# Optimization experiments

Hardware: AMD Instinct MI355X
Metric: run time of the kernel (lower is better)

Reference implementation:

```python
import jax, jax.numpy as jnp
import numpy as np


def euler_xyz_to_matrix(angles):
    # pytorch3d euler_angles_to_matrix(angles, 'XYZ') = R_X(a0) @ R_Y(a1) @ R_Z(a2)
    ax, ay, az = angles[..., 0], angles[..., 1], angles[..., 2]
    cx, sx = jnp.cos(ax), jnp.sin(ax)
    cy, sy = jnp.cos(ay), jnp.sin(ay)
    cz, sz = jnp.cos(az), jnp.sin(az)
    one = jnp.ones_like(ax)
    zero = jnp.zeros_like(ax)
    Rx = jnp.stack([one, zero, zero, zero, cx, -sx, zero, sx, cx], axis=-1).reshape(*ax.shape, 3, 3)
    Ry = jnp.stack([cy, zero, sy, zero, one, zero, -sy, zero, cy], axis=-1).reshape(*ax.shape, 3, 3)
    Rz = jnp.stack([cz, -sz, zero, sz, cz, zero, zero, zero, one], axis=-1).reshape(*ax.shape, 3, 3)
    return Rx @ Ry @ Rz


def chamfer_bidir(x, y):
    # x, y: [R, I, N, 3]. Squared-distance chamfer, mean point reduction, per (R,I) batch.
    x2 = jnp.sum(x * x, axis=-1)  # [R,I,N]
    y2 = jnp.sum(y * y, axis=-1)  # [R,I,N]
    # d2[r,i,n,m] = |x_n - y_m|^2
    d2 = x2[..., :, None] + y2[..., None, :] - 2.0 * jnp.einsum('rind,rimd->rinm', x, y)
    cham_x = jnp.mean(jnp.min(d2, axis=-1), axis=-1)  # x -> nearest y
    cham_y = jnp.mean(jnp.min(d2, axis=-2), axis=-1)  # y -> nearest x
    return cham_x + cham_y  # [R, I]


def setup_inputs() -> dict:
    key = jax.random.key(0)
    k1, k2, k3, k4 = jax.random.split(key, 4)
    R, I, N = 4, 16, 2048
    source_points = jax.random.normal(k1, (R, I, N, 3), dtype=jnp.float32)
    target_points = jax.random.normal(k2, (I, N, 3), dtype=jnp.float32)
    rotation = 0.1 * jax.random.normal(k3, (R, I, 3), dtype=jnp.float32)
    translation = 0.1 * jax.random.normal(k4, (R, I, 3), dtype=jnp.float32)
    scale = jnp.ones((R, I), dtype=jnp.float32)
    return {
        'source_points': source_points,
        'target_points': target_points,
        'rotation': rotation,
        'translation': translation,
        'scale': scale,
    }


def reference(source_points, target_points, rotation, translation, scale):
    R, I, N, _ = source_points.shape
    rot = euler_xyz_to_matrix(rotation)  # [R,I,3,3]
    # Transform per original: 4x4 matrix with rows [:3,:] scaled by `scale`,
    # so p' = scale * (rot @ p + translation).
    transformed = scale[..., None, None] * (
        jnp.einsum('rind,rikd->rink', source_points, rot) + translation[..., None, :]
    )  # [R,I,N,3]
    # target_points [I,N,3] broadcast to [R,I,N,3] (original repeats along R)
    target = jnp.broadcast_to(target_points[None], transformed.shape)
    # original calls chamfer_distance(target, transformed): x=target, y=transformed
    return chamfer_bidir(target, transformed)  # [R, I]
```

## Files before the change

kernel.cpp:

```cpp
#include <hip/hip_runtime.h>
#include <math.h>

#define RDIM 4
#define IDIM 16
#define NPAIR 64
#define NPTS 2048
#define THREADS 256
#define ROWSB 256
#define RBLK (NPTS / ROWSB)
#define TILES (NPTS / 32)
#define PSPLIT 4
#define ONEBF 0x3F80u

typedef __attribute__((ext_vector_type(8))) short bf16x8;
typedef __attribute__((ext_vector_type(16))) float f32x16;
typedef __attribute__((ext_vector_type(4))) float f32x4;

__device__ __forceinline__ float min3f(float a, float b, float c) {
    return fminf(a, fminf(b, c));
}

__device__ __forceinline__ unsigned int f2bf(float f) {
    union { float f; unsigned int u; } v; v.f = f;
    return (v.u + 0x7FFFu + ((v.u >> 16) & 1u)) >> 16;
}
__device__ __forceinline__ float bf2f(unsigned int h) {
    union { unsigned int u; float f; } v; v.u = h << 16; return v.f;
}

__device__ __forceinline__ void make_rot(const float* __restrict__ rotv, int pair,
                                         float& r00, float& r01, float& r02,
                                         float& r10, float& r11, float& r12,
                                         float& r20, float& r21, float& r22) {
    const float ax = rotv[pair * 3 + 0];
    const float ay = rotv[pair * 3 + 1];
    const float az = rotv[pair * 3 + 2];
    float sx, cx, sy, cy, sz, cz;
    sincosf(ax, &sx, &cx);
    sincosf(ay, &sy, &cy);
    sincosf(az, &sz, &cz);
    r00 = cy * cz;                r01 = -cy * sz;               r02 = sy;
    r10 = cx * sz + sx * sy * cz; r11 = cx * cz - sx * sy * sz; r12 = -sx * cy;
    r20 = sx * sz - cx * sy * cz; r21 = sx * cz + cx * sy * sz; r22 = cx * cy;
}

__device__ __forceinline__ uint4 brec(float v0, float v1, float v2) {
    const float b0 = -2.0f * v0, b1 = -2.0f * v1, b2 = -2.0f * v2;
    const unsigned int h0 = f2bf(b0), h1 = f2bf(b1), h2 = f2bf(b2);
    const unsigned int l0 = f2bf(b0 - bf2f(h0));
    const unsigned int l1 = f2bf(b1 - bf2f(h1));
    const unsigned int l2 = f2bf(b2 - bf2f(h2));
    const float n2 = v0 * v0 + v1 * v1 + v2 * v2;
    const unsigned int nh = f2bf(n2), nl = f2bf(n2 - bf2f(nh));
    return make_uint4(h0 | (h1 << 16), h2 | (l0 << 16), l1 | (l2 << 16), nh | (nl << 16));
}
__device__ __forceinline__ void arec(float q0, float q1, float q2, uint4& a0, uint4& a1) {
    const unsigned int h0 = f2bf(q0), h1 = f2bf(q1), h2 = f2bf(q2);
    const unsigned int l0 = f2bf(q0 - bf2f(h0));
    const unsigned int l1 = f2bf(q1 - bf2f(h1));
    const unsigned int l2 = f2bf(q2 - bf2f(h2));
    a0 = make_uint4(h0 | (h1 << 16), h2 | (l0 << 16), l1 | (l2 << 16), ONEBF);
    a1 = make_uint4(l0 | (l1 << 16), l2 | (h0 << 16), h1 | (h2 << 16), ONEBF << 16);
}

__global__ __launch_bounds__(THREADS)
void prep(const float* __restrict__ src, const float* __restrict__ tgt,
          const float* __restrict__ rotv, const float* __restrict__ trav,
          const float* __restrict__ scal,
          uint4* __restrict__ Yb, uint4* __restrict__ Ya,
          uint4* __restrict__ Xb, uint4* __restrict__ Xa,
          float* __restrict__ out)
{
    const int b   = blockIdx.x;
    const int seg = blockIdx.y;
    const int tid = threadIdx.x;
    if (b == 0 && seg == 0 && tid < NPAIR) out[tid] = 0.0f;
    const int m0  = seg * (NPTS / PSPLIT);
    if (b < NPAIR) {
        const int pair = b;
        float r00, r01, r02, r10, r11, r12, r20, r21, r22;
        make_rot(rotv, pair, r00, r01, r02, r10, r11, r12, r20, r21, r22);
        const float t0 = trav[pair * 3 + 0];
        const float t1 = trav[pair * 3 + 1];
        const float t2 = trav[pair * 3 + 2];
        const float s  = scal[pair];
        const float* __restrict__ srcp = src + (size_t)pair * NPTS * 3;
#pragma unroll
        for (int u = 0; u < NPTS / THREADS / PSPLIT; ++u) {
            const int m = m0 + u * THREADS + tid;
            const float p0 = srcp[m * 3 + 0];
            const float p1 = srcp[m * 3 + 1];
            const float p2 = srcp[m * 3 + 2];
            const float y0 = s * fmaf(r00, p0, fmaf(r01, p1, fmaf(r02, p2, t0)));
            const float y1 = s * fmaf(r10, p0, fmaf(r11, p1, fmaf(r12, p2, t1)));
            const float y2 = s * fmaf(r20, p0, fmaf(r21, p1, fmaf(r22, p2, t2)));
            Yb[(size_t)pair * NPTS + m] = brec(y0, y1, y2);
            uint4 a0, a1;
            arec(y0, y1, y2, a0, a1);
            Ya[((size_t)pair * NPTS + m) * 2 + 0] = a0;
            Ya[((size_t)pair * NPTS + m) * 2 + 1] = a1;
        }
    } else {
        const int i = b - NPAIR;
        const float* __restrict__ tgtp = tgt + (size_t)i * NPTS * 3;
#pragma unroll
        for (int u = 0; u < NPTS / THREADS / PSPLIT; ++u) {
            const int m = m0 + u * THREADS + tid;
            const float x0 = tgtp[m * 3 + 0];
            const float x1 = tgtp[m * 3 + 1];
            const float x2 = tgtp[m * 3 + 2];
            Xb[(size_t)i * NPTS + m] = brec(x0, x1, x2);
            uint4 a0, a1;
            arec(x0, x1, x2, a0, a1);
            Xa[((size_t)i * NPTS + m) * 2 + 0] = a0;
            Xa[((size_t)i * NPTS + m) * 2 + 1] = a1;
        }
    }
}

__global__ __launch_bounds__(THREADS, 3)
void chamfer_main(const uint4* __restrict__ Yb, const uint4* __restrict__ Ya,
                  const uint4* __restrict__ Xb, const uint4* __restrict__ Xa,
                  float* __restrict__ out, const float czero)
{
    __shared__ alignas(16) unsigned char smem[32768];
    __shared__ float rowmin[ROWSB];
    __shared__ float wsum[4];
    unsigned short* sB = (unsigned short*)smem;

    const int pair  = blockIdx.x;
    const int rb    = blockIdx.y;
    const int passB = blockIdx.z;
    const int i     = pair & (IDIM - 1);
    const int tid   = threadIdx.x;
    const int lane  = tid & 63;
    const int w     = tid >> 6;
    const int c31   = lane & 31;
    const int h     = lane >> 5;

    const uint4* __restrict__ gB = (passB == 0) ? (Yb + (size_t)pair * NPTS)
                                                : (Xb + (size_t)i * NPTS);
    const uint4* __restrict__ gA = (passB == 0)
        ? (Xa + ((size_t)i * NPTS + rb * ROWSB) * 2)
        : (Ya + ((size_t)pair * NPTS + rb * ROWSB) * 2);
    const char* gAb = (const char*)gA;

#pragma unroll
    for (int j = 0; j < 8; ++j)
        ((uint4*)sB)[j * THREADS + tid] = gB[j * THREADS + tid];

    const bf16x8 af0 = *(const bf16x8*)(gAb + (w * 64 + c31) * 32 + h * 16);
    const bf16x8 af1 = *(const bf16x8*)(gAb + (w * 64 + 32 + c31) * 32 + h * 16);

    f32x16 czv;
#pragma unroll
    for (int j = 0; j < 16; ++j) czv[j] = czero;

    float mn0[16], mn1[16];
#pragma unroll
    for (int j = 0; j < 16; ++j) { mn0[j] = 3.4e38f; mn1[j] = 3.4e38f; }

    __syncthreads();

    bf16x8 bfA = *(const bf16x8*)&sB[(0 * 32 + c31) * 8];
    bf16x8 bfB = *(const bf16x8*)&sB[(1 * 32 + c31) * 8];
    f32x16 a0  = __builtin_amdgcn_mfma_f32_32x32x16_bf16(af0, bfA, czv, 0, 0, 0);
    f32x16 b0  = __builtin_amdgcn_mfma_f32_32x32x16_bf16(af0, bfB, czv, 0, 0, 0);
    f32x16 pa1 = __builtin_amdgcn_mfma_f32_32x32x16_bf16(af1, bfA, czv, 0, 0, 0);
    f32x16 pb1 = __builtin_amdgcn_mfma_f32_32x32x16_bf16(af1, bfB, czv, 0, 0, 0);
#pragma unroll
    for (int j = 0; j < 16; ++j)
        mn0[j] = min3f(mn0[j], a0[j], b0[j]);

    for (int t = 2; t < TILES; t += 2) {
        bfA = *(const bf16x8*)&sB[((t + 0) * 32 + c31) * 8];
        bfB = *(const bf16x8*)&sB[((t + 1) * 32 + c31) * 8];
        a0 = __builtin_amdgcn_mfma_f32_32x32x16_bf16(af0, bfA, czv, 0, 0, 0);
        b0 = __builtin_amdgcn_mfma_f32_32x32x16_bf16(af0, bfB, czv, 0, 0, 0);
#pragma unroll
        for (int j = 0; j < 16; ++j)
            mn1[j] = min3f(mn1[j], pa1[j], pb1[j]);
        pa1 = __builtin_amdgcn_mfma_f32_32x32x16_bf16(af1, bfA, czv, 0, 0, 0);
        pb1 = __builtin_amdgcn_mfma_f32_32x32x16_bf16(af1, bfB, czv, 0, 0, 0);
#pragma unroll
        for (int j = 0; j < 16; ++j)
            mn0[j] = min3f(mn0[j], a0[j], b0[j]);
    }
#pragma unroll
    for (int j = 0; j < 16; ++j)
        mn1[j] = min3f(mn1[j], pa1[j], pb1[j]);

#pragma unroll
    for (int j = 0; j < 16; ++j) {
        float v0 = mn0[j], v1 = mn1[j];
        v0 = fminf(v0, __shfl_xor(v0, 1, 64));
        v1 = fminf(v1, __shfl_xor(v1, 1, 64));
        v0 = fminf(v0, __shfl_xor(v0, 2, 64));
        v1 = fminf(v1, __shfl_xor(v1, 2, 64));
        v0 = fminf(v0, __shfl_xor(v0, 4, 64));
        v1 = fminf(v1, __shfl_xor(v1, 4, 64));
        v0 = fminf(v0, __shfl_xor(v0, 8, 64));
        v1 = fminf(v1, __shfl_xor(v1, 8, 64));
        v0 = fminf(v0, __shfl_xor(v0, 16, 64));
        v1 = fminf(v1, __shfl_xor(v1, 16, 64));
        mn0[j] = v0; mn1[j] = v1;
    }

    if (c31 == 0) {
#pragma unroll
        for (int g = 0; g < 4; ++g) {
            f32x4 v4, u4;
            v4[0] = mn0[g * 4 + 0]; v4[1] = mn0[g * 4 + 1];
            v4[2] = mn0[g * 4 + 2]; v4[3] = mn0[g * 4 + 3];
            u4[0] = mn1[g * 4 + 0]; u4[1] = mn1[g * 4 + 1];
            u4[2] = mn1[g * 4 + 2]; u4[3] = mn1[g * 4 + 3];
            *(f32x4*)&rowmin[w * 64 + 8 * g + 4 * h] = v4;
            *(f32x4*)&rowmin[w * 64 + 32 + 8 * g + 4 * h] = u4;
        }
    }
    __syncthreads();

    const float m = rowmin[tid];
    const unsigned short* ar = (const unsigned short*)(gAb + tid * 32);
    const float q0 = bf2f(ar[0]) + bf2f(ar[3]);
    const float q1 = bf2f(ar[1]) + bf2f(ar[4]);
    const float q2 = bf2f(ar[2]) + bf2f(ar[5]);
    float v = m + q0 * q0 + q1 * q1 + q2 * q2;

#pragma unroll
    for (int off = 32; off > 0; off >>= 1)
        v += __shfl_down(v, off, 64);
    if (lane == 0) wsum[w] = v;
    __syncthreads();
    if (tid == 0) {
        const float tot = wsum[0] + wsum[1] + wsum[2] + wsum[3];
        atomicAdd(&out[pair], tot * (1.0f / NPTS));
    }
}

extern "C" void kernel_launch(void* const* d_in, const int* in_sizes, int n_in,
                              void* d_out, int out_size, void* d_ws, size_t ws_size,
                              hipStream_t stream) {
    const float* src  = (const float*)d_in[0];
    const float* tgt  = (const float*)d_in[1];
    const float* rotv = (const float*)d_in[2];
    const float* trav = (const float*)d_in[3];
    const float* scal = (const float*)d_in[4];
    float* out = (float*)d_out;

    char* ws = (char*)d_ws;
    uint4* Yb = (uint4*)ws;
    uint4* Ya = (uint4*)(ws + (size_t)NPAIR * NPTS * 16);
    uint4* Xb = (uint4*)(ws + (size_t)NPAIR * NPTS * 48);
    uint4* Xa = (uint4*)(ws + (size_t)NPAIR * NPTS * 48 + (size_t)IDIM * NPTS * 16);

    dim3 pgrid(NPAIR + IDIM, PSPLIT);
    prep<<<pgrid, THREADS, 0, stream>>>(src, tgt, rotv, trav, scal, Yb, Ya, Xb, Xa, out);

    dim3 grid(NPAIR, RBLK, 2);
    chamfer_main<<<grid, THREADS, 0, stream>>>(Yb, Ya, Xb, Xa, out, 0.0f);
}
```

Baseline: 85.79 us.

## Compute both chamfer directions from one distance pass with column atomicMin

Replaces the two-pass chamfer, which computed the distance matrix once per direction, with a single MFMA pass per block. That pass takes row minima in registers and column minima via shared-memory atomicMin on order-preserving uint keys, then merges the column minima into global memory with atomicMin. A third kernel reduces the column minima into the output. The x-norm is folded into the MFMA accumulator input instead of added afterwards, and the prep kernel stops writing the unused encodings. This halves the matrix work but adds per-tile cross-lane reductions, many shared and global atomics, an extra launch, and lower occupancy (launch bounds 3→2).

```diff
diff --git a/kernel.cpp b/kernel.cpp
--- a/kernel.cpp
+++ b/kernel.cpp
@@ -18,6 +18,15 @@
 
 __device__ __forceinline__ float min3f(float a, float b, float c) {
     return fminf(a, fminf(b, c));
+}
+
+__device__ __forceinline__ unsigned int fkey(float f) {
+    const unsigned int u = __float_as_uint(f);
+    return (u & 0x80000000u) ? ~u : (u | 0x80000000u);
+}
+__device__ __forceinline__ float funkey(unsigned int k) {
+    const unsigned int u = (k & 0x80000000u) ? (k ^ 0x80000000u) : ~k;
+    return __uint_as_float(u);
 }
 
 __device__ __forceinline__ unsigned int f2bf(float f) {
@@ -67,8 +76,8 @@
 void prep(const float* __restrict__ src, const float* __restrict__ tgt,
           const float* __restrict__ rotv, const float* __restrict__ trav,
           const float* __restrict__ scal,
-          uint4* __restrict__ Yb, uint4* __restrict__ Ya,
-          uint4* __restrict__ Xb, uint4* __restrict__ Xa,
+          uint4* __restrict__ Yb, uint4* __restrict__ Xa,
+          unsigned int* __restrict__ colminU,
           float* __restrict__ out)
 {
     const int b   = blockIdx.x;
@@ -78,6 +87,8 @@
     const int m0  = seg * (NPTS / PSPLIT);
     if (b < NPAIR) {
         const int pair = b;
+        colminU[(size_t)pair * NPTS + m0 + tid * 2 + 0] = 0xFFFFFFFFu;
+        colminU[(size_t)pair * NPTS + m0 + tid * 2 + 1] = 0xFFFFFFFFu;
         float r00, r01, r02, r10, r11, r12, r20, r21, r22;
         make_rot(rotv, pair, r00, r01, r02, r10, r11, r12, r20, r21, r22);
         const float t0 = trav[pair * 3 + 0];
@@ -95,10 +106,6 @@
             const float y1 = s * fmaf(r10, p0, fmaf(r11, p1, fmaf(r12, p2, t1)));
             const float y2 = s * fmaf(r20, p0, fmaf(r21, p1, fmaf(r22, p2, t2)));
             Yb[(size_t)pair * NPTS + m] = brec(y0, y1, y2);
-            uint4 a0, a1;
-            arec(y0, y1, y2, a0, a1);
-            Ya[((size_t)pair * NPTS + m) * 2 + 0] = a0;
-            Ya[((size_t)pair * NPTS + m) * 2 + 1] = a1;
         }
     } else {
         const int i = b - NPAIR;
@@ -109,7 +116,6 @@
             const float x0 = tgtp[m * 3 + 0];
             const float x1 = tgtp[m * 3 + 1];
             const float x2 = tgtp[m * 3 + 2];
-            Xb[(size_t)i * NPTS + m] = brec(x0, x1, x2);
             uint4 a0, a1;
             arec(x0, x1, x2, a0, a1);
             Xa[((size_t)i * NPTS + m) * 2 + 0] = a0;
@@ -118,19 +124,20 @@
     }
 }
 
-__global__ __launch_bounds__(THREADS, 3)
-void chamfer_main(const uint4* __restrict__ Yb, const uint4* __restrict__ Ya,
-                  const uint4* __restrict__ Xb, const uint4* __restrict__ Xa,
-                  float* __restrict__ out, const float czero)
+__global__ __launch_bounds__(THREADS, 2)
+void chamfer_main(const uint4* __restrict__ Yb, const uint4* __restrict__ Xa,
+                  unsigned int* __restrict__ colminU,
+                  float* __restrict__ out)
 {
     __shared__ alignas(16) unsigned char smem[32768];
+    __shared__ unsigned int colpartU[NPTS];
+    __shared__ float sx[ROWSB];
     __shared__ float rowmin[ROWSB];
     __shared__ float wsum[4];
     unsigned short* sB = (unsigned short*)smem;
 
     const int pair  = blockIdx.x;
     const int rb    = blockIdx.y;
-    const int passB = blockIdx.z;
     const int i     = pair & (IDIM - 1);
     const int tid   = threadIdx.x;
     const int lane  = tid & 63;
@@ -138,57 +145,69 @@
     const int c31   = lane & 31;
     const int h     = lane >> 5;
 
-    const uint4* __restrict__ gB = (passB == 0) ? (Yb + (size_t)pair * NPTS)
-                                                : (Xb + (size_t)i * NPTS);
-    const uint4* __restrict__ gA = (passB == 0)
-        ? (Xa + ((size_t)i * NPTS + rb * ROWSB) * 2)
-        : (Ya + ((size_t)pair * NPTS + rb * ROWSB) * 2);
-    const char* gAb = (const char*)gA;
+    const uint4* __restrict__ gB = Yb + (size_t)pair * NPTS;
+    const char* gAb = (const char*)(Xa + ((size_t)i * NPTS + rb * ROWSB) * 2);
 
 #pragma unroll
     for (int j = 0; j < 8; ++j)
         ((uint4*)sB)[j * THREADS + tid] = gB[j * THREADS + tid];
+#pragma unroll
+    for (int k = 0; k < 8; ++k)
+        colpartU[k * THREADS + tid] = 0xFFFFFFFFu;
+    {
+        const unsigned short* ar = (const unsigned short*)(gAb + tid * 32);
+        const float q0 = bf2f(ar[0]) + bf2f(ar[3]);
+        const float q1 = bf2f(ar[1]) + bf2f(ar[4]);
+        const float q2 = bf2f(ar[2]) + bf2f(ar[5]);
+        sx[tid] = q0 * q0 + q1 * q1 + q2 * q2;
+    }
 
     const bf16x8 af0 = *(const bf16x8*)(gAb + (w * 64 + c31) * 32 + h * 16);
     const bf16x8 af1 = *(const bf16x8*)(gAb + (w * 64 + 32 + c31) * 32 + h * 16);
 
-    f32x16 czv;
-#pragma unroll
-    for (int j = 0; j < 16; ++j) czv[j] = czero;
+    __syncthreads();
+
+    f32x16 cx0, cx1;
+#pragma unroll
+    for (int j = 0; j < 16; ++j) {
+        const int r = (j & 3) + 8 * (j >> 2) + 4 * h;
+        cx0[j] = sx[w * 64 + r];
+        cx1[j] = sx[w * 64 + 32 + r];
+    }
 
     float mn0[16], mn1[16];
 #pragma unroll
     for (int j = 0; j < 16; ++j) { mn0[j] = 3.4e38f; mn1[j] = 3.4e38f; }
-
-    __syncthreads();
 
     bf16x8 bfA = *(const bf16x8*)&sB[(0 * 32 + c31) * 8];
     bf16x8 bfB = *(const bf16x8*)&sB[(1 * 32 + c31) * 8];
-    f32x16 a0  = __builtin_amdgcn_mfma_f32_32x32x16_bf16(af0, bfA, czv, 0, 0, 0);
-    f32x16 b0  = __builtin_amdgcn_mfma_f32_32x32x16_bf16(af0, bfB, czv, 0, 0, 0);
-    f32x16 pa1 = __builtin_amdgcn_mfma_f32_32x32x16_bf16(af1, bfA, czv, 0, 0, 0);
-    f32x16 pb1 = __builtin_amdgcn_mfma_f32_32x32x16_bf16(af1, bfB, czv, 0, 0, 0);
-#pragma unroll
-    for (int j = 0; j < 16; ++j)
-        mn0[j] = min3f(mn0[j], a0[j], b0[j]);
-
-    for (int t = 2; t < TILES; t += 2) {
-        bfA = *(const bf16x8*)&sB[((t + 0) * 32 + c31) * 8];
-        bfB = *(const bf16x8*)&sB[((t + 1) * 32 + c31) * 8];
-        a0 = __builtin_amdgcn_mfma_f32_32x32x16_bf16(af0, bfA, czv, 0, 0, 0);
-        b0 = __builtin_amdgcn_mfma_f32_32x32x16_bf16(af0, bfB, czv, 0, 0, 0);
-#pragma unroll
-        for (int j = 0; j < 16; ++j)
-            mn1[j] = min3f(mn1[j], pa1[j], pb1[j]);
-        pa1 = __builtin_amdgcn_mfma_f32_32x32x16_bf16(af1, bfA, czv, 0, 0, 0);
-        pb1 = __builtin_amdgcn_mfma_f32_32x32x16_bf16(af1, bfB, czv, 0, 0, 0);
-#pragma unroll
-        for (int j = 0; j < 16; ++j)
+    for (int t = 0; t < TILES; t += 2) {
+        const f32x16 a0 = __builtin_amdgcn_mfma_f32_32x32x16_bf16(af0, bfA, cx0, 0, 0, 0);
+        const f32x16 a1 = __builtin_amdgcn_mfma_f32_32x32x16_bf16(af1, bfA, cx1, 0, 0, 0);
+        const f32x16 b0 = __builtin_amdgcn_mfma_f32_32x32x16_bf16(af0, bfB, cx0, 0, 0, 0);
+        const f32x16 b1 = __builtin_amdgcn_mfma_f32_32x32x16_bf16(af1, bfB, cx1, 0, 0, 0);
+        bfA = *(const bf16x8*)&sB[((((t + 2) & 63)) * 32 + c31) * 8];
+        bfB = *(const bf16x8*)&sB[((((t + 3) & 63)) * 32 + c31) * 8];
+#pragma unroll
+        for (int j = 0; j < 16; ++j) {
             mn0[j] = min3f(mn0[j], a0[j], b0[j]);
-    }
-#pragma unroll
-    for (int j = 0; j < 16; ++j)
-        mn1[j] = min3f(mn1[j], pa1[j], pb1[j]);
+            mn1[j] = min3f(mn1[j], a1[j], b1[j]);
+        }
+        float ca = fminf(a0[0], a1[0]);
+        float cb = fminf(b0[0], b1[0]);
+#pragma unroll
+        for (int j = 1; j < 16; ++j) {
+            ca = min3f(ca, a0[j], a1[j]);
+            cb = min3f(cb, b0[j], b1[j]);
+        }
+        ca = fminf(ca, __shfl_xor(ca, 32, 64));
+        cb = fminf(cb, __shfl_xor(cb, 32, 64));
+        if (h == 0) {
+            atomicMin(&colpartU[(t + 0) * 32 + c31], fkey(ca));
+            atomicMin(&colpartU[(t + 1) * 32 + c31], fkey(cb));
+        }
+    }
+    __syncthreads();
 
 #pragma unroll
     for (int j = 0; j < 16; ++j) {
@@ -205,7 +224,6 @@
         v1 = fminf(v1, __shfl_xor(v1, 16, 64));
         mn0[j] = v0; mn1[j] = v1;
     }
-
     if (c31 == 0) {
 #pragma unroll
         for (int g = 0; g < 4; ++g) {
@@ -218,19 +236,44 @@
             *(f32x4*)&rowmin[w * 64 + 32 + 8 * g + 4 * h] = u4;
         }
     }
-    __syncthreads();
-
-    const float m = rowmin[tid];
-    const unsigned short* ar = (const unsigned short*)(gAb + tid * 32);
-    const float q0 = bf2f(ar[0]) + bf2f(ar[3]);
-    const float q1 = bf2f(ar[1]) + bf2f(ar[4]);
-    const float q2 = bf2f(ar[2]) + bf2f(ar[5]);
-    float v = m + q0 * q0 + q1 * q1 + q2 * q2;
-
+
+#pragma unroll
+    for (int k = 0; k < 8; ++k) {
+        const int col = k * THREADS + tid;
+        atomicMin(&colminU[(size_t)pair * NPTS + col], colpartU[col]);
+    }
+    __syncthreads();
+
+    float v = rowmin[tid];
 #pragma unroll
     for (int off = 32; off > 0; off >>= 1)
         v += __shfl_down(v, off, 64);
     if (lane == 0) wsum[w] = v;
+    __syncthreads();
+    if (tid == 0) {
+        const float tot = wsum[0] + wsum[1] + wsum[2] + wsum[3];
+        atomicAdd(&out[pair], tot * (1.0f / NPTS));
+    }
+}
+
+__global__ __launch_bounds__(THREADS)
+void chamfer_col(const unsigned int* __restrict__ colminU, float* __restrict__ out)
+{
+    __shared__ float wsum[4];
+    const int pair = blockIdx.x;
+    const int tid  = threadIdx.x;
+    const int lane = tid & 63;
+    const int w    = tid >> 6;
+    float s = 0.0f;
+#pragma unroll
+    for (int k = 0; k < 8; ++k) {
+        const int col = k * THREADS + tid;
+        s += funkey(colminU[(size_t)pair * NPTS + col]);
+    }
+#pragma unroll
+    for (int off = 32; off > 0; off >>= 1)
+        s += __shfl_down(s, off, 64);
+    if (lane == 0) wsum[w] = s;
     __syncthreads();
     if (tid == 0) {
         const float tot = wsum[0] + wsum[1] + wsum[2] + wsum[3];
@@ -250,13 +293,15 @@
 
     char* ws = (char*)d_ws;
     uint4* Yb = (uint4*)ws;
-    uint4* Ya = (uint4*)(ws + (size_t)NPAIR * NPTS * 16);
-    uint4* Xb = (uint4*)(ws + (size_t)NPAIR * NPTS * 48);
-    uint4* Xa = (uint4*)(ws + (size_t)NPAIR * NPTS * 48 + (size_t)IDIM * NPTS * 16);
+    uint4* Xa = (uint4*)(ws + (size_t)NPAIR * NPTS * 16);
+    unsigned int* colminU = (unsigned int*)(ws + (size_t)NPAIR * NPTS * 16
+                                               + (size_t)IDIM * NPTS * 32);
 
     dim3 pgrid(NPAIR + IDIM, PSPLIT);
-    prep<<<pgrid, THREADS, 0, stream>>>(src, tgt, rotv, trav, scal, Yb, Ya, Xb, Xa, out);
-
-    dim3 grid(NPAIR, RBLK, 2);
-    chamfer_main<<<grid, THREADS, 0, stream>>>(Yb, Ya, Xb, Xa, out, 0.0f);
-}
+    prep<<<pgrid, THREADS, 0, stream>>>(src, tgt, rotv, trav, scal, Yb, Xa, colminU, out);
+
+    dim3 grid(NPAIR, RBLK);
+    chamfer_main<<<grid, THREADS, 0, stream>>>(Yb, Xa, colminU, out);
+
+    chamfer_col<<<NPAIR, THREADS, 0, stream>>>(colminU, out);
+}
```

Result: slower. 95.12 us (+10.9%).
